# Performance work log

Hardware: AMD Instinct MI355X
Metric: run time of the kernel (lower is better)

## Reference

```python
import jax, jax.numpy as jnp
import numpy as np

NUM_CLASSES = 5
B, D, H, W = 4, 64, 256, 256


def _per_class_counts(labels, weights, num_classes):
    # labels: [B, N] int, weights: [B, N] float -> [B, C] float counts
    b = labels.shape[0]
    ids = labels + jnp.arange(b, dtype=labels.dtype)[:, None] * num_classes
    counts = jax.ops.segment_sum(weights.ravel(), ids.ravel().astype(jnp.int32),
                                 num_segments=b * num_classes)
    return counts.reshape(b, num_classes)


def _dice(predicted, target, num_classes):
    b = predicted.shape[0]
    p = predicted.reshape(b, -1)  # [B, N] integer class labels
    t = target.reshape(b, -1)
    ones = jnp.ones(p.shape, dtype=jnp.float32)
    pred_sum = _per_class_counts(p, ones, num_classes)                      # sum of one-hot(pred) over voxels
    tar_sum = _per_class_counts(t, ones, num_classes)                       # sum of one-hot(target) over voxels
    inter = _per_class_counts(p, (p == t).astype(jnp.float32), num_classes) # per-class intersection counts
    num = 2.0 * inter
    den = pred_sum + tar_sum
    zero = den == 0
    num = jnp.where(zero, 1.0, num)
    den = jnp.where(zero, 1.0, den)
    return (num / den).mean(axis=0)  # [C]


def setup_inputs() -> dict:
    key = jax.random.key(0)
    k1, k2 = jax.random.split(key)
    predicted = jax.random.randint(k1, (B, D, H, W), 0, NUM_CLASSES, dtype=jnp.int32)
    target = jax.random.randint(k2, (B, D, H, W), 0, NUM_CLASSES, dtype=jnp.int32)
    return {"predicted": predicted, "target": target}


def reference(predicted, target):
    return _dice(predicted, target, NUM_CLASSES)
```

## Files before the change

### kernel.cpp

```cpp
#include <hip/hip_runtime.h>

#define NUM_CLASSES 5
#define BATCH 4
#define NPB (64 * 256 * 256)
#define VEC_PER_BATCH (NPB / 4)
#define THREADS 256
#define VECS 16
#define CHUNK 8
#define BLOCKS_X (VEC_PER_BATCH / (THREADS * VECS))
#define SLOTS 15
#define PSTRIDE 16


__global__ __launch_bounds__(THREADS, 4) void dice_count_kernel(
    const int* __restrict__ pred, const int* __restrict__ targ,
    unsigned int* __restrict__ partial) {
  const int b = blockIdx.y;
  const int4* __restrict__ p4 = (const int4*)(pred + (long long)b * NPB);
  const int4* __restrict__ t4 = (const int4*)(targ + (long long)b * NPB);

  const int base = blockIdx.x * (THREADS * VECS) + threadIdx.x;

  unsigned accP[2] = {0, 0}, accT[2] = {0, 0}, accI[2] = {0, 0};

#pragma unroll
  for (int h = 0; h < 2; ++h) {
    int4 pv[CHUNK], tv[CHUNK];
#pragma unroll
    for (int k = 0; k < CHUNK; ++k) {
      const int idx = base + (h * CHUNK + k) * THREADS;
      pv[k] = p4[idx];
      tv[k] = t4[idx];
    }
    __builtin_amdgcn_sched_barrier(0);
    unsigned aP = 0, aT = 0, aI = 0;
#define ACC_ELEM(PE, TE)                               \
    {                                                  \
      const unsigned op = 1u << (6u * (unsigned)(PE)); \
      aP += op;                                        \
      aT += 1u << (6u * (unsigned)(TE));               \
      aI += ((PE) == (TE)) ? op : 0u;                  \
    }
#pragma unroll
    for (int k = 0; k < CHUNK; ++k) {
      ACC_ELEM(pv[k].x, tv[k].x)
      ACC_ELEM(pv[k].y, tv[k].y)
      ACC_ELEM(pv[k].z, tv[k].z)
      ACC_ELEM(pv[k].w, tv[k].w)
    }
    accP[h] = aP; accT[h] = aT; accI[h] = aI;
  }

#define UNPACK(A, R01, R23, R4)                                          \
  unsigned R01 = ((A[0] & 63u) + (A[1] & 63u)) |                         \
                 ((((A[0] >> 6) & 63u) + ((A[1] >> 6) & 63u)) << 16);    \
  unsigned R23 = (((A[0] >> 12) & 63u) + ((A[1] >> 12) & 63u)) |         \
                 ((((A[0] >> 18) & 63u) + ((A[1] >> 18) & 63u)) << 16);  \
  unsigned R4 = ((A[0] >> 24) & 63u) + ((A[1] >> 24) & 63u);
  UNPACK(accP, p01, p23, p4r)
  UNPACK(accT, t01, t23, t4r)
  UNPACK(accI, i01, i23, i4r)

#pragma unroll
  for (int off = 32; off >= 1; off >>= 1) {
    p01 += (unsigned)__shfl_xor((int)p01, off);
    p23 += (unsigned)__shfl_xor((int)p23, off);
    p4r += (unsigned)__shfl_xor((int)p4r, off);
    t01 += (unsigned)__shfl_xor((int)t01, off);
    t23 += (unsigned)__shfl_xor((int)t23, off);
    t4r += (unsigned)__shfl_xor((int)t4r, off);
    i01 += (unsigned)__shfl_xor((int)i01, off);
    i23 += (unsigned)__shfl_xor((int)i23, off);
    i4r += (unsigned)__shfl_xor((int)i4r, off);
  }

  __shared__ unsigned int s[SLOTS];
  if (threadIdx.x < SLOTS) s[threadIdx.x] = 0;
  __syncthreads();

  if ((threadIdx.x & 63) == 0) {
    atomicAdd(&s[0], p01 & 0xFFFFu);
    atomicAdd(&s[1], p01 >> 16);
    atomicAdd(&s[2], p23 & 0xFFFFu);
    atomicAdd(&s[3], p23 >> 16);
    atomicAdd(&s[4], p4r);
    atomicAdd(&s[5], t01 & 0xFFFFu);
    atomicAdd(&s[6], t01 >> 16);
    atomicAdd(&s[7], t23 & 0xFFFFu);
    atomicAdd(&s[8], t23 >> 16);
    atomicAdd(&s[9], t4r);
    atomicAdd(&s[10], i01 & 0xFFFFu);
    atomicAdd(&s[11], i01 >> 16);
    atomicAdd(&s[12], i23 & 0xFFFFu);
    atomicAdd(&s[13], i23 >> 16);
    atomicAdd(&s[14], i4r);
  }
  __syncthreads();

  if (threadIdx.x < SLOTS)
    partial[(b * BLOCKS_X + blockIdx.x) * PSTRIDE + threadIdx.x] = s[threadIdx.x];
}

__global__ __launch_bounds__(256) void dice_final_kernel(
    const unsigned int* __restrict__ partial, float* __restrict__ out) {
  __shared__ unsigned int red[BATCH * SLOTS][4];
  const int t = threadIdx.x;
  if (t < BATCH * SLOTS * 4) {
    const int q = t & 3;
    const int s = (t >> 2) % SLOTS;
    const int bb = (t >> 2) / SLOTS;
    unsigned int sum = 0;
    for (int j = q * (BLOCKS_X / 4); j < (q + 1) * (BLOCKS_X / 4); ++j)
      sum += partial[(bb * BLOCKS_X + j) * PSTRIDE + s];
    red[(t >> 2)][q] = sum;
  }
  __syncthreads();
  if (t < NUM_CLASSES) {
    float acc = 0.0f;
#pragma unroll
    for (int bb = 0; bb < BATCH; ++bb) {
      const int ip = bb * SLOTS + t;
      const int it = bb * SLOTS + 5 + t;
      const int ii = bb * SLOTS + 10 + t;
      const float ps = (float)(red[ip][0] + red[ip][1] + red[ip][2] + red[ip][3]);
      const float ts = (float)(red[it][0] + red[it][1] + red[it][2] + red[it][3]);
      const float is = (float)(red[ii][0] + red[ii][1] + red[ii][2] + red[ii][3]);
      float num = 2.0f * is;
      float den = ps + ts;
      if (den == 0.0f) { num = 1.0f; den = 1.0f; }
      acc += num / den;
    }
    out[t] = acc * (1.0f / BATCH);
  }
}

extern "C" void kernel_launch(void* const* d_in, const int* in_sizes, int n_in,
                              void* d_out, int out_size, void* d_ws, size_t ws_size,
                              hipStream_t stream) {
  const int* pred = (const int*)d_in[0];
  const int* targ = (const int*)d_in[1];
  float* out = (float*)d_out;
  unsigned int* partial = (unsigned int*)d_ws;

  dim3 grid(BLOCKS_X, BATCH);
  dice_count_kernel<<<grid, THREADS, 0, stream>>>(pred, targ, partial);
  dice_final_kernel<<<1, 256, 0, stream>>>(partial, out);
}
```

Baseline: 148.3 us.

## Fuse final reduction into count kernel via global atomics and last-block ticket

```diff
diff --git a/kernel.cpp b/kernel.cpp
--- a/kernel.cpp
+++ b/kernel.cpp
@@ -8,13 +8,16 @@
 #define VECS 16
 #define CHUNK 8
 #define BLOCKS_X (VEC_PER_BATCH / (THREADS * VECS))
+#define NBLOCKS (BLOCKS_X * BATCH)
 #define SLOTS 15
-#define PSTRIDE 16
+#define ACC_STRIDE 16
+#define TICKET_IDX (BATCH * SLOTS * ACC_STRIDE)
+#define WS_WORDS (TICKET_IDX + ACC_STRIDE)
 
 
-__global__ __launch_bounds__(THREADS, 4) void dice_count_kernel(
+__global__ __launch_bounds__(THREADS, 4) void dice_fused_kernel(
     const int* __restrict__ pred, const int* __restrict__ targ,
-    unsigned int* __restrict__ partial) {
+    unsigned int* __restrict__ ws, float* __restrict__ out) {
   const int b = blockIdx.y;
   const int4* __restrict__ p4 = (const int4*)(pred + (long long)b * NPB);
   const int4* __restrict__ t4 = (const int4*)(targ + (long long)b * NPB);
@@ -75,6 +78,7 @@
   }
 
   __shared__ unsigned int s[SLOTS];
+  __shared__ unsigned int done;
   if (threadIdx.x < SLOTS) s[threadIdx.x] = 0;
   __syncthreads();
 
@@ -97,40 +101,38 @@
   }
   __syncthreads();
 
-  if (threadIdx.x < SLOTS)
-    partial[(b * BLOCKS_X + blockIdx.x) * PSTRIDE + threadIdx.x] = s[threadIdx.x];
-}
-
-__global__ __launch_bounds__(256) void dice_final_kernel(
-    const unsigned int* __restrict__ partial, float* __restrict__ out) {
-  __shared__ unsigned int red[BATCH * SLOTS][4];
-  const int t = threadIdx.x;
-  if (t < BATCH * SLOTS * 4) {
-    const int q = t & 3;
-    const int s = (t >> 2) % SLOTS;
-    const int bb = (t >> 2) / SLOTS;
-    unsigned int sum = 0;
-    for (int j = q * (BLOCKS_X / 4); j < (q + 1) * (BLOCKS_X / 4); ++j)
-      sum += partial[(bb * BLOCKS_X + j) * PSTRIDE + s];
-    red[(t >> 2)][q] = sum;
+  if (threadIdx.x < SLOTS) {
+    atomicAdd(&ws[(b * SLOTS + threadIdx.x) * ACC_STRIDE], s[threadIdx.x]);
+    __threadfence();
   }
   __syncthreads();
-  if (t < NUM_CLASSES) {
-    float acc = 0.0f;
+
+  if (threadIdx.x == 0) done = atomicAdd(&ws[TICKET_IDX], 1u);
+  __syncthreads();
+
+  if (done == NBLOCKS - 1) {
+    __threadfence();
+    __shared__ float red[BATCH * SLOTS];
+    if (threadIdx.x < BATCH * SLOTS) {
+      unsigned v = atomicAdd(&ws[threadIdx.x * ACC_STRIDE], 0u);
+      red[threadIdx.x] = (float)v;
+    }
+    __syncthreads();
+    if (threadIdx.x < NUM_CLASSES) {
+      const int t = threadIdx.x;
+      float acc = 0.0f;
 #pragma unroll
-    for (int bb = 0; bb < BATCH; ++bb) {
-      const int ip = bb * SLOTS + t;
-      const int it = bb * SLOTS + 5 + t;
-      const int ii = bb * SLOTS + 10 + t;
-      const float ps = (float)(red[ip][0] + red[ip][1] + red[ip][2] + red[ip][3]);
-      const float ts = (float)(red[it][0] + red[it][1] + red[it][2] + red[it][3]);
-      const float is = (float)(red[ii][0] + red[ii][1] + red[ii][2] + red[ii][3]);
-      float num = 2.0f * is;
-      float den = ps + ts;
-      if (den == 0.0f) { num = 1.0f; den = 1.0f; }
-      acc += num / den;
+      for (int bb = 0; bb < BATCH; ++bb) {
+        const float ps = red[bb * SLOTS + t];
+        const float ts = red[bb * SLOTS + 5 + t];
+        const float is = red[bb * SLOTS + 10 + t];
+        float num = 2.0f * is;
+        float den = ps + ts;
+        if (den == 0.0f) { num = 1.0f; den = 1.0f; }
+        acc += num / den;
+      }
+      out[t] = acc * (1.0f / BATCH);
     }
-    out[t] = acc * (1.0f / BATCH);
   }
 }
 
@@ -140,9 +142,10 @@
   const int* pred = (const int*)d_in[0];
   const int* targ = (const int*)d_in[1];
   float* out = (float*)d_out;
-  unsigned int* partial = (unsigned int*)d_ws;
+  unsigned int* ws = (unsigned int*)d_ws;
+
+  hipMemsetAsync(d_ws, 0, WS_WORDS * sizeof(unsigned int), stream);
 
   dim3 grid(BLOCKS_X, BATCH);
-  dice_count_kernel<<<grid, THREADS, 0, stream>>>(pred, targ, partial);
-  dice_final_kernel<<<1, 256, 0, stream>>>(partial, out);
+  dice_fused_kernel<<<grid, THREADS, 0, stream>>>(pred, targ, ws, out);
 }
```

Measured after the change: 197.9 us. +33.5%, slower.

## Shrink per-block work and aggregate partials via global atomics into rows

Applied to the files above, without the earlier changes.

```diff
diff --git a/kernel.cpp b/kernel.cpp
--- a/kernel.cpp
+++ b/kernel.cpp
@@ -5,11 +5,13 @@
 #define NPB (64 * 256 * 256)
 #define VEC_PER_BATCH (NPB / 4)
 #define THREADS 256
-#define VECS 16
-#define CHUNK 8
+#define VECS 4
 #define BLOCKS_X (VEC_PER_BATCH / (THREADS * VECS))
+#define BLOCKS_PER_ROW 4
+#define ROWS_X (BLOCKS_X / BLOCKS_PER_ROW)
 #define SLOTS 15
 #define PSTRIDE 16
+#define WS_BYTES (BATCH * ROWS_X * PSTRIDE * 4)
 
 
 __global__ __launch_bounds__(THREADS, 4) void dice_count_kernel(
@@ -21,19 +23,14 @@
 
   const int base = blockIdx.x * (THREADS * VECS) + threadIdx.x;
 
-  unsigned accP[2] = {0, 0}, accT[2] = {0, 0}, accI[2] = {0, 0};
+  int4 pv[VECS], tv[VECS];
+#pragma unroll
+  for (int k = 0; k < VECS; ++k) {
+    pv[k] = p4[base + k * THREADS];
+    tv[k] = t4[base + k * THREADS];
+  }
 
-#pragma unroll
-  for (int h = 0; h < 2; ++h) {
-    int4 pv[CHUNK], tv[CHUNK];
-#pragma unroll
-    for (int k = 0; k < CHUNK; ++k) {
-      const int idx = base + (h * CHUNK + k) * THREADS;
-      pv[k] = p4[idx];
-      tv[k] = t4[idx];
-    }
-    __builtin_amdgcn_sched_barrier(0);
-    unsigned aP = 0, aT = 0, aI = 0;
+  unsigned aP = 0, aT = 0, aI = 0;
 #define ACC_ELEM(PE, TE)                               \
     {                                                  \
       const unsigned op = 1u << (6u * (unsigned)(PE)); \
@@ -42,24 +39,20 @@
       aI += ((PE) == (TE)) ? op : 0u;                  \
     }
 #pragma unroll
-    for (int k = 0; k < CHUNK; ++k) {
-      ACC_ELEM(pv[k].x, tv[k].x)
-      ACC_ELEM(pv[k].y, tv[k].y)
-      ACC_ELEM(pv[k].z, tv[k].z)
-      ACC_ELEM(pv[k].w, tv[k].w)
-    }
-    accP[h] = aP; accT[h] = aT; accI[h] = aI;
+  for (int k = 0; k < VECS; ++k) {
+    ACC_ELEM(pv[k].x, tv[k].x)
+    ACC_ELEM(pv[k].y, tv[k].y)
+    ACC_ELEM(pv[k].z, tv[k].z)
+    ACC_ELEM(pv[k].w, tv[k].w)
   }
 
-#define UNPACK(A, R01, R23, R4)                                          \
-  unsigned R01 = ((A[0] & 63u) + (A[1] & 63u)) |                         \
-                 ((((A[0] >> 6) & 63u) + ((A[1] >> 6) & 63u)) << 16);    \
-  unsigned R23 = (((A[0] >> 12) & 63u) + ((A[1] >> 12) & 63u)) |         \
-                 ((((A[0] >> 18) & 63u) + ((A[1] >> 18) & 63u)) << 16);  \
-  unsigned R4 = ((A[0] >> 24) & 63u) + ((A[1] >> 24) & 63u);
-  UNPACK(accP, p01, p23, p4r)
-  UNPACK(accT, t01, t23, t4r)
-  UNPACK(accI, i01, i23, i4r)
+#define UNPACK(A, R01, R23, R4)                        \
+  unsigned R01 = (A & 63u) | (((A >> 6) & 63u) << 16); \
+  unsigned R23 = ((A >> 12) & 63u) | (((A >> 18) & 63u) << 16); \
+  unsigned R4 = (A >> 24) & 63u;
+  UNPACK(aP, p01, p23, p4r)
+  UNPACK(aT, t01, t23, t4r)
+  UNPACK(aI, i01, i23, i4r)
 
 #pragma unroll
   for (int off = 32; off >= 1; off >>= 1) {
@@ -97,8 +90,9 @@
   }
   __syncthreads();
 
+  const int row = b * ROWS_X + (blockIdx.x >> 2);
   if (threadIdx.x < SLOTS)
-    partial[(b * BLOCKS_X + blockIdx.x) * PSTRIDE + threadIdx.x] = s[threadIdx.x];
+    atomicAdd(&partial[row * PSTRIDE + threadIdx.x], s[threadIdx.x]);
 }
 
 __global__ __launch_bounds__(256) void dice_final_kernel(
@@ -110,8 +104,8 @@
     const int s = (t >> 2) % SLOTS;
     const int bb = (t >> 2) / SLOTS;
     unsigned int sum = 0;
-    for (int j = q * (BLOCKS_X / 4); j < (q + 1) * (BLOCKS_X / 4); ++j)
-      sum += partial[(bb * BLOCKS_X + j) * PSTRIDE + s];
+    for (int j = q * (ROWS_X / 4); j < (q + 1) * (ROWS_X / 4); ++j)
+      sum += partial[(bb * ROWS_X + j) * PSTRIDE + s];
     red[(t >> 2)][q] = sum;
   }
   __syncthreads();
@@ -142,6 +136,8 @@
   float* out = (float*)d_out;
   unsigned int* partial = (unsigned int*)d_ws;
 
+  hipMemsetAsync(d_ws, 0, WS_BYTES, stream);
+
   dim3 grid(BLOCKS_X, BATCH);
   dice_count_kernel<<<grid, THREADS, 0, stream>>>(pred, targ, partial);
   dice_final_kernel<<<1, 256, 0, stream>>>(partial, out);
```

After: 149.4 us. About the same (+0.8%).
